# Kernel tuning notes

Hardware: AMD Instinct MI355X
Metric: run time of the kernel (lower is better)

## Reference

```python
import jax, jax.numpy as jnp
import numpy as np
import math

EMBED_DIM = 1024
NUM_HEADS = 16
HEAD_DIM = EMBED_DIM // NUM_HEADS
BLOCK = 64  # hardcoded block_size in the original
SCALE = 1.0 / math.sqrt(HEAD_DIM)


def setup_inputs() -> dict:
    key = jax.random.key(0)
    ks = jax.random.split(key, 6)
    B, S, E = 4, 2048, EMBED_DIM
    std = 1.0 / math.sqrt(E)
    return {
        "x": jax.random.normal(ks[0], (B, S, E), dtype=jnp.float32),
        "q_w": jax.random.normal(ks[1], (E, E), dtype=jnp.float32) * std,
        "k_w": jax.random.normal(ks[2], (E, E), dtype=jnp.float32) * std,
        "v_w": jax.random.normal(ks[3], (E, E), dtype=jnp.float32) * std,
        "out_w": jax.random.normal(ks[4], (E, E), dtype=jnp.float32) * std,
        "out_b": jnp.zeros((E,), dtype=jnp.float32),
    }


def _flash_attn(Q, K, V):
    # Q,K,V: [B,H,S,hd]. Faithful to the torch loop: outer loop over KEY blocks i,
    # inner vectorized over all query rows. Reproduces the original's buggy
    # softmax_sum update (overwrites instead of accumulating the running sum).
    B, H, S, hd = Q.shape
    nkb = S // BLOCK
    Kb = K.reshape(B, H, nkb, BLOCK, hd).transpose(2, 0, 1, 3, 4)  # [nkb,B,H,bs,hd]
    Vb = V.reshape(B, H, nkb, BLOCK, hd).transpose(2, 0, 1, 3, 4)

    out0 = jnp.zeros_like(Q)
    m0 = jnp.full((B, H, S, 1), -jnp.inf, dtype=Q.dtype)
    l0 = jnp.zeros((B, H, S, 1), dtype=Q.dtype)

    def body(carry, kv):
        out, m, l = carry
        K_blk, V_blk = kv  # [B,H,bs,hd]
        scores = jnp.einsum('bhqd,bhkd->bhqk', Q, K_blk) * SCALE  # [B,H,S,bs]
        M_ij = scores.max(axis=-1, keepdims=True)
        m_new = jnp.maximum(m, M_ij)
        corr = jnp.exp(m - m_new)
        exp_scores = jnp.exp(scores - m_new)
        chunk_sum = exp_scores.sum(axis=-1, keepdims=True)
        l_new = chunk_sum * corr + chunk_sum  # BUG preserved from original
        out_new = out * corr + jnp.einsum('bhqk,bhkd->bhqd', exp_scores, V_blk)
        return (out_new, m_new, l_new), None

    (out, m, l), _ = jax.lax.scan(body, (out0, m0, l0), (Kb, Vb))
    return out / l


def reference(x, q_w, k_w, v_w, out_w, out_b):
    B, S, E = x.shape
    H, hd = NUM_HEADS, HEAD_DIM

    def split_heads(t):
        return t.reshape(B, S, H, hd).transpose(0, 2, 1, 3)  # [B,H,S,hd]

    Q = split_heads(x @ q_w.T)
    K = split_heads(x @ k_w.T)
    V = split_heads(x @ v_w.T)

    out = _flash_attn(Q, K, V)  # [B,H,S,hd]
    out = out.transpose(0, 2, 1, 3).reshape(B, S, E)
    return out @ out_w.T + out_b
```

## Files before the change

### kernel.cpp

```cpp
#include <hip/hip_runtime.h>
#include <math.h>

#define EDIM 1024
#define SEQ  2048
#define NB   4
#define NH   16
#define HD   64
#define NKB  32
#define QSC2 0.18033688011112042f

#define KVT_BYTES 24576
#define QT_BYTES  16384

typedef _Float16 half8  __attribute__((ext_vector_type(8)));
typedef _Float16 half4v __attribute__((ext_vector_type(4)));
typedef float    f32x4  __attribute__((ext_vector_type(4)));

#define MFMA16(a, b, c) __builtin_amdgcn_mfma_f32_16x16x32_f16((a), (b), (c), 0, 0, 0)

__device__ __forceinline__ void split4(const float4 v, half4v* hi, half4v* lo) {
    _Float16 h0 = (_Float16)v.x, h1 = (_Float16)v.y,
             h2 = (_Float16)v.z, h3 = (_Float16)v.w;
    half4v h; h[0] = h0; h[1] = h1; h[2] = h2; h[3] = h3;
    half4v l;
    l[0] = (_Float16)(v.x - (float)h0);
    l[1] = (_Float16)(v.y - (float)h1);
    l[2] = (_Float16)(v.z - (float)h2);
    l[3] = (_Float16)(v.w - (float)h3);
    *hi = h; *lo = l;
}

__device__ __forceinline__ void gemm_core(const float* __restrict__ X,
                                          const float* __restrict__ W,
                                          int row_m, int row_n,
                                          _Float16* Ah, _Float16* Al,
                                          _Float16* Bh, _Float16* Bl,
                                          f32x4 acc[4][4])
{
    const int t    = threadIdx.x;
    const int lane = t & 63;
    const int wave = t >> 6;
    const int wm   = (wave >> 1) * 64, wn = (wave & 1) * 64;
    const int l15  = lane & 15, l4 = lane >> 4;

    const int srow = t >> 1;
    const int sc16 = (t & 1) * 16;

    const float* Xp = X + (size_t)(row_m + srow) * EDIM + sc16;
    const float* Wp = W + (size_t)(row_n + srow) * EDIM + sc16;

    float4 xa[4], wa[4];
    #pragma unroll
    for (int j = 0; j < 4; ++j) {
        xa[j] = *(const float4*)(Xp + 4 * j);
        wa[j] = *(const float4*)(Wp + 4 * j);
    }

    const f32x4 zz = {0.f, 0.f, 0.f, 0.f};
    #pragma unroll
    for (int m = 0; m < 4; ++m)
        #pragma unroll
        for (int n = 0; n < 4; ++n) acc[m][n] = zz;

    for (int kt = 0; kt < EDIM / 32; ++kt) {
        __syncthreads();
        #pragma unroll
        for (int j = 0; j < 4; ++j) {
            const int col = sc16 + 4 * j;
            const int idx = srow * 32 + (((col >> 3) ^ (srow & 3)) << 3) + (col & 7);
            half4v hi, lo;
            split4(xa[j], &hi, &lo);
            *(half4v*)(Ah + idx) = hi; *(half4v*)(Al + idx) = lo;
            split4(wa[j], &hi, &lo);
            *(half4v*)(Bh + idx) = hi; *(half4v*)(Bl + idx) = lo;
        }
        if (kt + 1 < EDIM / 32) {
            #pragma unroll
            for (int j = 0; j < 4; ++j) {
                xa[j] = *(const float4*)(Xp + (kt + 1) * 32 + 4 * j);
                wa[j] = *(const float4*)(Wp + (kt + 1) * 32 + 4 * j);
            }
        }
        __syncthreads();

        half8 ah[4], al[4];
        #pragma unroll
        for (int m = 0; m < 4; ++m) {
            const int row  = wm + m * 16 + l15;
            const int slot = l4 ^ (row & 3);
            ah[m] = *(const half8*)(Ah + row * 32 + slot * 8);
            al[m] = *(const half8*)(Al + row * 32 + slot * 8);
        }
        #pragma unroll
        for (int n = 0; n < 4; ++n) {
            const int row  = wn + n * 16 + l15;
            const int slot = l4 ^ (row & 3);
            half8 bh = *(const half8*)(Bh + row * 32 + slot * 8);
            half8 bl = *(const half8*)(Bl + row * 32 + slot * 8);
            #pragma unroll
            for (int m = 0; m < 4; ++m) {
                acc[m][n] = MFMA16(ah[m], bh, acc[m][n]);
                acc[m][n] = MFMA16(ah[m], bl, acc[m][n]);
                acc[m][n] = MFMA16(al[m], bh, acc[m][n]);
            }
        }
    }
}

__global__ __launch_bounds__(256)
void qkv_mfma(const float* __restrict__ X,
              const float* __restrict__ Wq, const float* __restrict__ Wk,
              const float* __restrict__ Wv,
              char* __restrict__ Qt, char* __restrict__ KVt)
{
    __shared__ __align__(16) _Float16 Ah[128 * 32], Al[128 * 32];
    __shared__ __align__(16) _Float16 Bh[128 * 32], Bl[128 * 32];

    const float* W = (blockIdx.z == 0) ? Wq : (blockIdx.z == 1) ? Wk : Wv;

    const int row_m = blockIdx.y * 128, row_n = blockIdx.x * 128;
    f32x4 acc[4][4];
    gemm_core(X, W, row_m, row_n, Ah, Al, Bh, Bl, acc);

    const int lane = threadIdx.x & 63, wave = threadIdx.x >> 6;
    const int wm = (wave >> 1) * 64, wn = (wave & 1) * 64;
    const int l15 = lane & 15, l4 = lane >> 4;

    const int b  = row_m >> 11;
    const int hh = (row_n + wn) >> 6;
    const int kb = ((row_m & 2047) + wm) >> 6;
    const size_t tile = ((size_t)b * NH + hh) * NKB + kb;

    if (blockIdx.z == 2) {
        char* vb = KVt + tile * KVT_BYTES + 16384;
        #pragma unroll
        for (int m = 0; m < 4; ++m) {
            const int slot_k = m * 2 + (l4 >> 1);
            const int koff   = (l4 & 1) * 8;
            #pragma unroll
            for (int n = 0; n < 4; ++n) {
                const int d = n * 16 + l15;
                half4v hv;
                #pragma unroll
                for (int r = 0; r < 4; ++r) hv[r] = (_Float16)acc[m][n][r];
                *(half4v*)(vb + d * 128 + ((slot_k ^ (d & 7)) << 4) + koff) = hv;
            }
        }
    } else {
        char* base = (blockIdx.z == 0) ? (Qt + tile * QT_BYTES)
                                       : (KVt + tile * KVT_BYTES);
        const float sc = (blockIdx.z == 0) ? QSC2 : 1.f;
        #pragma unroll
        for (int m = 0; m < 4; ++m)
            #pragma unroll
            for (int r = 0; r < 4; ++r) {
                const int row = m * 16 + l4 * 4 + r;
                const int rb  = row * 128;
                #pragma unroll
                for (int n = 0; n < 4; ++n) {
                    const int byte = rb + (((2 * n + (l15 >> 3)) ^ (row & 7)) << 4)
                                   + (l15 & 7) * 2;
                    const float v = acc[m][n][r] * sc;
                    const _Float16 hi = (_Float16)v;
                    *(_Float16*)(base + byte)        = hi;
                    *(_Float16*)(base + 8192 + byte) = (_Float16)(v - (float)hi);
                }
            }
    }
}

__global__ __launch_bounds__(256)
void out_mfma(const float* __restrict__ X, const float* __restrict__ W,
              const float* __restrict__ bias, float* __restrict__ O)
{
    __shared__ __align__(16) _Float16 Ah[128 * 32], Al[128 * 32];
    __shared__ __align__(16) _Float16 Bh[128 * 32], Bl[128 * 32];

    const int row_m = blockIdx.y * 128, row_n = blockIdx.x * 128;
    f32x4 acc[4][4];
    gemm_core(X, W, row_m, row_n, Ah, Al, Bh, Bl, acc);

    const int lane = threadIdx.x & 63, wave = threadIdx.x >> 6;
    const int wm = (wave >> 1) * 64, wn = (wave & 1) * 64;
    const int l15 = lane & 15, l4 = lane >> 4;
    #pragma unroll
    for (int m = 0; m < 4; ++m) {
        #pragma unroll
        for (int r = 0; r < 4; ++r) {
            const int R = row_m + wm + m * 16 + l4 * 4 + r;
            #pragma unroll
            for (int n = 0; n < 4; ++n) {
                const int C = row_n + wn + n * 16 + l15;
                O[(size_t)R * EDIM + C] = acc[m][n][r] + bias[C];
            }
        }
    }
}

__device__ __forceinline__ void stage_tile(const char* g, char* lds,
                                           int wave, int lane)
{
    #pragma unroll
    for (int i = 0; i < 6; ++i) {
        __builtin_amdgcn_global_load_lds(
            (const __attribute__((address_space(1))) void*)(g + wave * 6144 + i * 1024 + lane * 16),
            (__attribute__((address_space(3))) void*)(lds + wave * 6144 + i * 1024),
            16, 0, 0);
    }
}

__global__ __launch_bounds__(256)
void attn_mfma(const char* __restrict__ Qt, const char* __restrict__ KVt,
               float* __restrict__ A)
{
    __shared__ __align__(16) char LDS[2 * KVT_BYTES];

    const int t    = threadIdx.x;
    const int lane = t & 63;
    const int wave = t >> 6;
    const int l15  = lane & 15, l4 = lane >> 4;

    const int wg   = blockIdx.x;
    const int xcd  = wg & 7;
    const int idx  = wg >> 3;
    const int pair = xcd * 8 + (idx >> 5);
    const int qt   = idx & 31;
    const int b    = pair >> 4;
    const int h    = pair & 15;

    const char* qg  = Qt  + (((size_t)b * NH + h) * NKB + qt) * QT_BYTES;
    const char* kvg = KVt + (((size_t)b * NH + h) * NKB) * (size_t)KVT_BYTES;

    half8 qfh[2], qfl[2];
    #pragma unroll
    for (int ds = 0; ds < 2; ++ds) {
        const int row  = wave * 16 + l15;
        const int slot = (ds * 4 + l4) ^ (row & 7);
        const int off  = row * 128 + slot * 16;
        qfh[ds] = *(const half8*)(qg + off);
        qfl[ds] = *(const half8*)(qg + 8192 + off);
    }

    int buf = 0;
    stage_tile(kvg, LDS, wave, lane);
    asm volatile("s_waitcnt vmcnt(0)" ::: "memory");
    __syncthreads();

    float m_run[4], l_run[4];
    #pragma unroll
    for (int r = 0; r < 4; ++r) { m_run[r] = -INFINITY; l_run[r] = 0.f; }
    const f32x4 zz = {0.f, 0.f, 0.f, 0.f};
    f32x4 oacc[4];
    #pragma unroll
    for (int nf = 0; nf < 4; ++nf) oacc[nf] = zz;

    for (int kb = 0; kb < NKB; ++kb) {
        char* cb = LDS + buf * KVT_BYTES;
        if (kb + 1 < NKB)
            stage_tile(kvg + (size_t)(kb + 1) * KVT_BYTES,
                       LDS + (buf ^ 1) * KVT_BYTES, wave, lane);

        f32x4 sacc[4];
        #pragma unroll
        for (int nf = 0; nf < 4; ++nf) sacc[nf] = zz;
        #pragma unroll
        for (int nf = 0; nf < 4; ++nf) {
            #pragma unroll
            for (int ds = 0; ds < 2; ++ds) {
                const int row  = nf * 16 + l15;
                const int slot = (ds * 4 + l4) ^ (row & 7);
                const int off  = row * 128 + slot * 16;
                half8 bh = *(const half8*)(cb + off);
                half8 bl = *(const half8*)(cb + 8192 + off);
                sacc[nf] = MFMA16(qfh[ds], bh, sacc[nf]);
                sacc[nf] = MFMA16(qfh[ds], bl, sacc[nf]);
                sacc[nf] = MFMA16(qfl[ds], bh, sacc[nf]);
            }
        }

        float corr[4], p[4][4];
        #pragma unroll
        for (int r = 0; r < 4; ++r) {
            float mx = fmaxf(fmaxf(sacc[0][r], sacc[1][r]),
                             fmaxf(sacc[2][r], sacc[3][r]));
            mx = fmaxf(mx, __shfl_xor(mx, 1));
            mx = fmaxf(mx, __shfl_xor(mx, 2));
            mx = fmaxf(mx, __shfl_xor(mx, 4));
            mx = fmaxf(mx, __shfl_xor(mx, 8));
            const float mnew = fmaxf(m_run[r], mx);
            corr[r]  = exp2f(m_run[r] - mnew);
            m_run[r] = mnew;
            float cs = 0.f;
            #pragma unroll
            for (int nf = 0; nf < 4; ++nf) {
                p[r][nf] = exp2f(sacc[nf][r] - mnew);
                cs += p[r][nf];
            }
            cs += __shfl_xor(cs, 1);
            cs += __shfl_xor(cs, 2);
            cs += __shfl_xor(cs, 4);
            cs += __shfl_xor(cs, 8);
            l_run[r] = cs * corr[r] + cs;
        }

        __syncthreads();

        #pragma unroll
        for (int r = 0; r < 4; ++r) {
            const int qrow = wave * 16 + l4 * 4 + r;
            const int rb   = qrow * 128;
            #pragma unroll
            for (int nf = 0; nf < 4; ++nf) {
                *(_Float16*)(cb + rb
                             + (((2 * nf + (l15 >> 3)) ^ (qrow & 7)) << 4)
                             + (l15 & 7) * 2) = (_Float16)p[r][nf];
            }
        }

        #pragma unroll
        for (int nf = 0; nf < 4; ++nf)
            #pragma unroll
            for (int r = 0; r < 4; ++r)
                oacc[nf][r] *= corr[r];

        half8 pa[2];
        #pragma unroll
        for (int ks = 0; ks < 2; ++ks) {
            const int row  = wave * 16 + l15;
            const int slot = (ks * 4 + l4) ^ (row & 7);
            pa[ks] = *(const half8*)(cb + row * 128 + slot * 16);
        }
        #pragma unroll
        for (int nf = 0; nf < 4; ++nf) {
            #pragma unroll
            for (int ks = 0; ks < 2; ++ks) {
                const int row  = nf * 16 + l15;
                const int slot = (ks * 4 + l4) ^ (row & 7);
                half8 vh = *(const half8*)(cb + 16384 + row * 128 + slot * 16);
                oacc[nf] = MFMA16(pa[ks], vh, oacc[nf]);
            }
        }

        asm volatile("s_waitcnt vmcnt(0)" ::: "memory");
        __syncthreads();
        buf ^= 1;
    }

    #pragma unroll
    for (int nf = 0; nf < 4; ++nf) {
        #pragma unroll
        for (int r = 0; r < 4; ++r) {
            const int qrow = qt * 64 + wave * 16 + l4 * 4 + r;
            const int d = nf * 16 + l15;
            A[((size_t)b * SEQ + qrow) * EDIM + h * HD + d] = oacc[nf][r] / l_run[r];
        }
    }
}

extern "C" void kernel_launch(void* const* d_in, const int* in_sizes, int n_in,
                              void* d_out, int out_size, void* d_ws, size_t ws_size,
                              hipStream_t stream)
{
    (void)in_sizes; (void)n_in; (void)out_size; (void)ws_size;
    const float* x  = (const float*)d_in[0];
    const float* qw = (const float*)d_in[1];
    const float* kw = (const float*)d_in[2];
    const float* vw = (const float*)d_in[3];
    const float* ow = (const float*)d_in[4];
    const float* ob = (const float*)d_in[5];
    float* out = (float*)d_out;

    char*  KVt = (char*)d_ws;
    char*  Qt  = KVt + (size_t)NB * NH * NKB * KVT_BYTES;
    float* Ab  = (float*)(Qt + (size_t)NB * NH * NKB * QT_BYTES);

    dim3 blk(256);
    qkv_mfma<<<dim3(EDIM / 128, (NB * SEQ) / 128, 3), blk, 0, stream>>>(
        x, qw, kw, vw, Qt, KVt);
    attn_mfma<<<dim3(NKB * NH * NB), blk, 0, stream>>>(Qt, KVt, Ab);
    out_mfma<<<dim3(EDIM / 128, (NB * SEQ) / 128, 1), blk, 0, stream>>>(
        Ab, ow, ob, out);
}
```

Measured before the change: 577.6 us.

## Drop lo-part split terms, enlarge attention query tile, compute row sums via MFMA

Drops the low-half correction term for activations in the projection GEMMs and for K in attention, cutting one of three MFMAs per product and shrinking LDS and KV tile storage. The attention kernel now processes 128 query rows per workgroup (two 16-row subtiles per wave), reusing each K/V fragment load across both. It moves P to a dedicated LDS buffer, computes row sums with an MFMA against a ones vector, and adds s_setprio around MFMA blocks. Precision drops because activation and K residuals are no longer included, which risks tolerance failures.

```diff
diff --git a/kernel.cpp b/kernel.cpp
--- a/kernel.cpp
+++ b/kernel.cpp
@@ -9,7 +9,7 @@
 #define NKB  32
 #define QSC2 0.18033688011112042f
 
-#define KVT_BYTES 24576
+#define KVT_BYTES 16384
 #define QT_BYTES  16384
 
 typedef _Float16 half8  __attribute__((ext_vector_type(8)));
@@ -30,10 +30,17 @@
     *hi = h; *lo = l;
 }
 
+__device__ __forceinline__ half4v hi4(const float4 v) {
+    half4v h;
+    h[0] = (_Float16)v.x; h[1] = (_Float16)v.y;
+    h[2] = (_Float16)v.z; h[3] = (_Float16)v.w;
+    return h;
+}
+
 __device__ __forceinline__ void gemm_core(const float* __restrict__ X,
                                           const float* __restrict__ W,
                                           int row_m, int row_n,
-                                          _Float16* Ah, _Float16* Al,
+                                          _Float16* Ah,
                                           _Float16* Bh, _Float16* Bl,
                                           f32x4 acc[4][4])
 {
@@ -68,9 +75,8 @@
         for (int j = 0; j < 4; ++j) {
             const int col = sc16 + 4 * j;
             const int idx = srow * 32 + (((col >> 3) ^ (srow & 3)) << 3) + (col & 7);
+            *(half4v*)(Ah + idx) = hi4(xa[j]);
             half4v hi, lo;
-            split4(xa[j], &hi, &lo);
-            *(half4v*)(Ah + idx) = hi; *(half4v*)(Al + idx) = lo;
             split4(wa[j], &hi, &lo);
             *(half4v*)(Bh + idx) = hi; *(half4v*)(Bl + idx) = lo;
         }
@@ -83,13 +89,12 @@
         }
         __syncthreads();
 
-        half8 ah[4], al[4];
+        half8 ah[4];
         #pragma unroll
         for (int m = 0; m < 4; ++m) {
             const int row  = wm + m * 16 + l15;
             const int slot = l4 ^ (row & 3);
             ah[m] = *(const half8*)(Ah + row * 32 + slot * 8);
-            al[m] = *(const half8*)(Al + row * 32 + slot * 8);
         }
         #pragma unroll
         for (int n = 0; n < 4; ++n) {
@@ -101,7 +106,6 @@
             for (int m = 0; m < 4; ++m) {
                 acc[m][n] = MFMA16(ah[m], bh, acc[m][n]);
                 acc[m][n] = MFMA16(ah[m], bl, acc[m][n]);
-                acc[m][n] = MFMA16(al[m], bh, acc[m][n]);
             }
         }
     }
@@ -113,14 +117,14 @@
               const float* __restrict__ Wv,
               char* __restrict__ Qt, char* __restrict__ KVt)
 {
-    __shared__ __align__(16) _Float16 Ah[128 * 32], Al[128 * 32];
+    __shared__ __align__(16) _Float16 Ah[128 * 32];
     __shared__ __align__(16) _Float16 Bh[128 * 32], Bl[128 * 32];
 
     const float* W = (blockIdx.z == 0) ? Wq : (blockIdx.z == 1) ? Wk : Wv;
 
     const int row_m = blockIdx.y * 128, row_n = blockIdx.x * 128;
     f32x4 acc[4][4];
-    gemm_core(X, W, row_m, row_n, Ah, Al, Bh, Bl, acc);
+    gemm_core(X, W, row_m, row_n, Ah, Bh, Bl, acc);
 
     const int lane = threadIdx.x & 63, wave = threadIdx.x >> 6;
     const int wm = (wave >> 1) * 64, wn = (wave & 1) * 64;
@@ -132,7 +136,7 @@
     const size_t tile = ((size_t)b * NH + hh) * NKB + kb;
 
     if (blockIdx.z == 2) {
-        char* vb = KVt + tile * KVT_BYTES + 16384;
+        char* vb = KVt + tile * KVT_BYTES + 8192;
         #pragma unroll
         for (int m = 0; m < 4; ++m) {
             const int slot_k = m * 2 + (l4 >> 1);
@@ -147,9 +151,9 @@
             }
         }
     } else {
-        char* base = (blockIdx.z == 0) ? (Qt + tile * QT_BYTES)
-                                       : (KVt + tile * KVT_BYTES);
-        const float sc = (blockIdx.z == 0) ? QSC2 : 1.f;
+        const bool isQ = (blockIdx.z == 0);
+        char* base = isQ ? (Qt + tile * QT_BYTES) : (KVt + tile * KVT_BYTES);
+        const float sc = isQ ? QSC2 : 1.f;
         #pragma unroll
         for (int m = 0; m < 4; ++m)
             #pragma unroll
@@ -162,8 +166,9 @@
                                    + (l15 & 7) * 2;
                     const float v = acc[m][n][r] * sc;
                     const _Float16 hi = (_Float16)v;
-                    *(_Float16*)(base + byte)        = hi;
-                    *(_Float16*)(base + 8192 + byte) = (_Float16)(v - (float)hi);
+                    *(_Float16*)(base + byte) = hi;
+                    if (isQ)
+                        *(_Float16*)(base + 8192 + byte) = (_Float16)(v - (float)hi);
                 }
             }
     }
@@ -173,12 +178,12 @@
 void out_mfma(const float* __restrict__ X, const float* __restrict__ W,
               const float* __restrict__ bias, float* __restrict__ O)
 {
-    __shared__ __align__(16) _Float16 Ah[128 * 32], Al[128 * 32];
+    __shared__ __align__(16) _Float16 Ah[128 * 32];
     __shared__ __align__(16) _Float16 Bh[128 * 32], Bl[128 * 32];
 
     const int row_m = blockIdx.y * 128, row_n = blockIdx.x * 128;
     f32x4 acc[4][4];
-    gemm_core(X, W, row_m, row_n, Ah, Al, Bh, Bl, acc);
+    gemm_core(X, W, row_m, row_n, Ah, Bh, Bl, acc);
 
     const int lane = threadIdx.x & 63, wave = threadIdx.x >> 6;
     const int wm = (wave >> 1) * 64, wn = (wave & 1) * 64;
@@ -197,14 +202,14 @@
     }
 }
 
-__device__ __forceinline__ void stage_tile(const char* g, char* lds,
-                                           int wave, int lane)
-{
-    #pragma unroll
-    for (int i = 0; i < 6; ++i) {
+__device__ __forceinline__ void stage_tile16(const char* g, char* lds,
+                                             int wave, int lane)
+{
+    #pragma unroll
+    for (int i = 0; i < 4; ++i) {
         __builtin_amdgcn_global_load_lds(
-            (const __attribute__((address_space(1))) void*)(g + wave * 6144 + i * 1024 + lane * 16),
-            (__attribute__((address_space(3))) void*)(lds + wave * 6144 + i * 1024),
+            (const __attribute__((address_space(1))) void*)(g + i * 4096 + wave * 1024 + lane * 16),
+            (__attribute__((address_space(3))) void*)(lds + i * 4096 + wave * 1024),
             16, 0, 0);
     }
 }
@@ -213,148 +218,180 @@
 void attn_mfma(const char* __restrict__ Qt, const char* __restrict__ KVt,
                float* __restrict__ A)
 {
-    __shared__ __align__(16) char LDS[2 * KVT_BYTES];
+    __shared__ __align__(16) char LDS[2 * KVT_BYTES + 16384];
 
     const int t    = threadIdx.x;
     const int lane = t & 63;
     const int wave = t >> 6;
     const int l15  = lane & 15, l4 = lane >> 4;
 
-    const int wg   = blockIdx.x;
-    const int xcd  = wg & 7;
-    const int idx  = wg >> 3;
-    const int pair = xcd * 8 + (idx >> 5);
-    const int qt   = idx & 31;
-    const int b    = pair >> 4;
-    const int h    = pair & 15;
-
-    const char* qg  = Qt  + (((size_t)b * NH + h) * NKB + qt) * QT_BYTES;
+    const int wg    = blockIdx.x;
+    const int xcd   = wg & 7;
+    const int idx   = wg >> 3;
+    const int pair  = xcd * 8 + (idx >> 4);
+    const int qt128 = idx & 15;
+    const int b     = pair >> 4;
+    const int h     = pair & 15;
+
+    const char* qg  = Qt  + (((size_t)b * NH + h) * NKB + qt128 * 2) * (size_t)QT_BYTES;
     const char* kvg = KVt + (((size_t)b * NH + h) * NKB) * (size_t)KVT_BYTES;
-
-    half8 qfh[2], qfl[2];
-    #pragma unroll
-    for (int ds = 0; ds < 2; ++ds) {
-        const int row  = wave * 16 + l15;
-        const int slot = (ds * 4 + l4) ^ (row & 7);
-        const int off  = row * 128 + slot * 16;
-        qfh[ds] = *(const half8*)(qg + off);
-        qfl[ds] = *(const half8*)(qg + 8192 + off);
-    }
+    char* Pb = LDS + 2 * KVT_BYTES;
+
+    const int q0 = wave * 32;
+
+    stage_tile16(kvg, LDS, wave, lane);
+
+    half8 qfh[2][2], qfl[2][2];
+    #pragma unroll
+    for (int qt = 0; qt < 2; ++qt) {
+        const int qr = q0 + qt * 16;
+        const char* qtile = qg + (qr >> 6) * QT_BYTES;
+        const int row = (qr & 63) + l15;
+        #pragma unroll
+        for (int ds = 0; ds < 2; ++ds) {
+            const int off = row * 128 + (((ds * 4 + l4) ^ (row & 7)) << 4);
+            qfh[qt][ds] = *(const half8*)(qtile + off);
+            qfl[qt][ds] = *(const half8*)(qtile + 8192 + off);
+        }
+    }
+
+    half8 ones;
+    #pragma unroll
+    for (int i = 0; i < 8; ++i) ones[i] = (_Float16)1.0f;
+
+    float m_run[2][4], l_run[2][4], corr[2][4];
+    #pragma unroll
+    for (int qt = 0; qt < 2; ++qt)
+        #pragma unroll
+        for (int r = 0; r < 4; ++r) { m_run[qt][r] = -INFINITY; l_run[qt][r] = 0.f; }
+
+    const f32x4 zz = {0.f, 0.f, 0.f, 0.f};
+    f32x4 oacc[2][4];
+    #pragma unroll
+    for (int qt = 0; qt < 2; ++qt)
+        #pragma unroll
+        for (int nf = 0; nf < 4; ++nf) oacc[qt][nf] = zz;
 
     int buf = 0;
-    stage_tile(kvg, LDS, wave, lane);
-    asm volatile("s_waitcnt vmcnt(0)" ::: "memory");
-    __syncthreads();
-
-    float m_run[4], l_run[4];
-    #pragma unroll
-    for (int r = 0; r < 4; ++r) { m_run[r] = -INFINITY; l_run[r] = 0.f; }
-    const f32x4 zz = {0.f, 0.f, 0.f, 0.f};
-    f32x4 oacc[4];
-    #pragma unroll
-    for (int nf = 0; nf < 4; ++nf) oacc[nf] = zz;
-
     for (int kb = 0; kb < NKB; ++kb) {
-        char* cb = LDS + buf * KVT_BYTES;
+        asm volatile("s_waitcnt vmcnt(0)" ::: "memory");
+        __syncthreads();
         if (kb + 1 < NKB)
-            stage_tile(kvg + (size_t)(kb + 1) * KVT_BYTES,
-                       LDS + (buf ^ 1) * KVT_BYTES, wave, lane);
-
-        f32x4 sacc[4];
-        #pragma unroll
-        for (int nf = 0; nf < 4; ++nf) sacc[nf] = zz;
+            stage_tile16(kvg + (size_t)(kb + 1) * KVT_BYTES,
+                         LDS + (buf ^ 1) * KVT_BYTES, wave, lane);
+
+        const char* cb = LDS + buf * KVT_BYTES;
+
+        f32x4 sacc[2][4];
+        #pragma unroll
+        for (int qt = 0; qt < 2; ++qt)
+            #pragma unroll
+            for (int nf = 0; nf < 4; ++nf) sacc[qt][nf] = zz;
+
+        __builtin_amdgcn_s_setprio(1);
         #pragma unroll
         for (int nf = 0; nf < 4; ++nf) {
             #pragma unroll
             for (int ds = 0; ds < 2; ++ds) {
                 const int row  = nf * 16 + l15;
                 const int slot = (ds * 4 + l4) ^ (row & 7);
-                const int off  = row * 128 + slot * 16;
-                half8 bh = *(const half8*)(cb + off);
-                half8 bl = *(const half8*)(cb + 8192 + off);
-                sacc[nf] = MFMA16(qfh[ds], bh, sacc[nf]);
-                sacc[nf] = MFMA16(qfh[ds], bl, sacc[nf]);
-                sacc[nf] = MFMA16(qfl[ds], bh, sacc[nf]);
-            }
-        }
-
-        float corr[4], p[4][4];
-        #pragma unroll
-        for (int r = 0; r < 4; ++r) {
-            float mx = fmaxf(fmaxf(sacc[0][r], sacc[1][r]),
-                             fmaxf(sacc[2][r], sacc[3][r]));
-            mx = fmaxf(mx, __shfl_xor(mx, 1));
-            mx = fmaxf(mx, __shfl_xor(mx, 2));
-            mx = fmaxf(mx, __shfl_xor(mx, 4));
-            mx = fmaxf(mx, __shfl_xor(mx, 8));
-            const float mnew = fmaxf(m_run[r], mx);
-            corr[r]  = exp2f(m_run[r] - mnew);
-            m_run[r] = mnew;
-            float cs = 0.f;
-            #pragma unroll
-            for (int nf = 0; nf < 4; ++nf) {
-                p[r][nf] = exp2f(sacc[nf][r] - mnew);
-                cs += p[r][nf];
-            }
-            cs += __shfl_xor(cs, 1);
-            cs += __shfl_xor(cs, 2);
-            cs += __shfl_xor(cs, 4);
-            cs += __shfl_xor(cs, 8);
-            l_run[r] = cs * corr[r] + cs;
-        }
-
-        __syncthreads();
-
-        #pragma unroll
-        for (int r = 0; r < 4; ++r) {
-            const int qrow = wave * 16 + l4 * 4 + r;
-            const int rb   = qrow * 128;
-            #pragma unroll
-            for (int nf = 0; nf < 4; ++nf) {
-                *(_Float16*)(cb + rb
-                             + (((2 * nf + (l15 >> 3)) ^ (qrow & 7)) << 4)
-                             + (l15 & 7) * 2) = (_Float16)p[r][nf];
-            }
-        }
-
-        #pragma unroll
-        for (int nf = 0; nf < 4; ++nf)
-            #pragma unroll
-            for (int r = 0; r < 4; ++r)
-                oacc[nf][r] *= corr[r];
-
-        half8 pa[2];
-        #pragma unroll
-        for (int ks = 0; ks < 2; ++ks) {
-            const int row  = wave * 16 + l15;
-            const int slot = (ks * 4 + l4) ^ (row & 7);
-            pa[ks] = *(const half8*)(cb + row * 128 + slot * 16);
-        }
+                half8 bh = *(const half8*)(cb + row * 128 + slot * 16);
+                #pragma unroll
+                for (int qt = 0; qt < 2; ++qt) {
+                    sacc[qt][nf] = MFMA16(qfh[qt][ds], bh, sacc[qt][nf]);
+                    sacc[qt][nf] = MFMA16(qfl[qt][ds], bh, sacc[qt][nf]);
+                }
+            }
+        }
+        __builtin_amdgcn_s_setprio(0);
+
+        #pragma unroll
+        for (int qt = 0; qt < 2; ++qt) {
+            #pragma unroll
+            for (int r = 0; r < 4; ++r) {
+                float mx = fmaxf(fmaxf(sacc[qt][0][r], sacc[qt][1][r]),
+                                 fmaxf(sacc[qt][2][r], sacc[qt][3][r]));
+                mx = fmaxf(mx, __shfl_xor(mx, 1));
+                mx = fmaxf(mx, __shfl_xor(mx, 2));
+                mx = fmaxf(mx, __shfl_xor(mx, 4));
+                mx = fmaxf(mx, __shfl_xor(mx, 8));
+                const float mnew = fmaxf(m_run[qt][r], mx);
+                corr[qt][r]  = exp2f(m_run[qt][r] - mnew);
+                m_run[qt][r] = mnew;
+                #pragma unroll
+                for (int nf = 0; nf < 4; ++nf)
+                    sacc[qt][nf][r] = exp2f(sacc[qt][nf][r] - mnew);
+            }
+        }
+
+        #pragma unroll
+        for (int qt = 0; qt < 2; ++qt)
+            #pragma unroll
+            for (int r = 0; r < 4; ++r) {
+                const int qrow = q0 + qt * 16 + l4 * 4 + r;
+                const int rb   = qrow * 128;
+                #pragma unroll
+                for (int nf = 0; nf < 4; ++nf)
+                    *(_Float16*)(Pb + rb
+                                 + (((2 * nf + (l15 >> 3)) ^ (qrow & 7)) << 4)
+                                 + (l15 & 7) * 2) = (_Float16)sacc[qt][nf][r];
+            }
+
+        half8 pa[2][2];
+        #pragma unroll
+        for (int qt = 0; qt < 2; ++qt) {
+            const int row = q0 + qt * 16 + l15;
+            #pragma unroll
+            for (int ks = 0; ks < 2; ++ks) {
+                const int slot = (ks * 4 + l4) ^ (row & 7);
+                pa[qt][ks] = *(const half8*)(Pb + row * 128 + slot * 16);
+            }
+        }
+
+        #pragma unroll
+        for (int qt = 0; qt < 2; ++qt) {
+            f32x4 lacc = zz;
+            lacc = MFMA16(pa[qt][0], ones, lacc);
+            lacc = MFMA16(pa[qt][1], ones, lacc);
+            #pragma unroll
+            for (int r = 0; r < 4; ++r) {
+                const float cs = lacc[r];
+                l_run[qt][r] = cs * corr[qt][r] + cs;
+                #pragma unroll
+                for (int nf = 0; nf < 4; ++nf)
+                    oacc[qt][nf][r] *= corr[qt][r];
+            }
+        }
+
+        __builtin_amdgcn_s_setprio(1);
         #pragma unroll
         for (int nf = 0; nf < 4; ++nf) {
             #pragma unroll
             for (int ks = 0; ks < 2; ++ks) {
                 const int row  = nf * 16 + l15;
                 const int slot = (ks * 4 + l4) ^ (row & 7);
-                half8 vh = *(const half8*)(cb + 16384 + row * 128 + slot * 16);
-                oacc[nf] = MFMA16(pa[ks], vh, oacc[nf]);
-            }
-        }
-
-        asm volatile("s_waitcnt vmcnt(0)" ::: "memory");
-        __syncthreads();
+                half8 vh = *(const half8*)(cb + 8192 + row * 128 + slot * 16);
+                #pragma unroll
+                for (int qt = 0; qt < 2; ++qt)
+                    oacc[qt][nf] = MFMA16(pa[qt][ks], vh, oacc[qt][nf]);
+            }
+        }
+        __builtin_amdgcn_s_setprio(0);
+
         buf ^= 1;
     }
 
     #pragma unroll
-    for (int nf = 0; nf < 4; ++nf) {
-        #pragma unroll
-        for (int r = 0; r < 4; ++r) {
-            const int qrow = qt * 64 + wave * 16 + l4 * 4 + r;
-            const int d = nf * 16 + l15;
-            A[((size_t)b * SEQ + qrow) * EDIM + h * HD + d] = oacc[nf][r] / l_run[r];
-        }
-    }
+    for (int qt = 0; qt < 2; ++qt)
+        #pragma unroll
+        for (int nf = 0; nf < 4; ++nf)
+            #pragma unroll
+            for (int r = 0; r < 4; ++r) {
+                const int qrow = qt128 * 128 + q0 + qt * 16 + l4 * 4 + r;
+                const int d = nf * 16 + l15;
+                A[((size_t)b * SEQ + qrow) * EDIM + h * HD + d] =
+                    oacc[qt][nf][r] / l_run[qt][r];
+            }
 }
 
 extern "C" void kernel_launch(void* const* d_in, const int* in_sizes, int n_in,
@@ -377,7 +414,7 @@
     dim3 blk(256);
     qkv_mfma<<<dim3(EDIM / 128, (NB * SEQ) / 128, 3), blk, 0, stream>>>(
         x, qw, kw, vw, Qt, KVt);
-    attn_mfma<<<dim3(NKB * NH * NB), blk, 0, stream>>>(Qt, KVt, Ab);
+    attn_mfma<<<dim3((SEQ / 128) * NH * NB), blk, 0, stream>>>(Qt, KVt, Ab);
     out_mfma<<<dim3(EDIM / 128, (NB * SEQ) / 128, 1), blk, 0, stream>>>(
         Ab, ow, ob, out);
 }
```

Result: faster. 486.0 us (-15.9%).
